# Kernel optimization log

Hardware: AMD Instinct MI355X
Metric: run time of the kernel (lower is better)

The kernel has to match this reference:

```python
import jax, jax.numpy as jnp
import numpy as np

N = 2048   # number of proposals
D = 128    # appearance feature dim
DK = 64    # key/query dim
DG = 64    # geometric embedding dim
SD = 8     # single relation output dim = appear_dim / N_r = 128/16


def setup_inputs() -> dict:
    key = jax.random.key(0)
    ks = jax.random.split(key, 10)
    s = jnp.float32(0.05)
    return {
        "appearance_feature": jax.random.normal(ks[0], (N, D), jnp.float32),
        "geometric_feature": jax.random.uniform(ks[1], (N, N, DG), jnp.float32),
        "Wv": jax.random.normal(ks[2], (D, SD), jnp.float32) * s,
        "bv": jnp.zeros((SD,), jnp.float32),
        "Wk": jax.random.normal(ks[3], (D, DK), jnp.float32) * s,
        "bk": jnp.zeros((DK,), jnp.float32),
        "Wq": jax.random.normal(ks[4], (D, DK), jnp.float32) * s,
        "bq": jnp.zeros((DK,), jnp.float32),
        "Wg": jax.random.normal(ks[5], (DG, 1), jnp.float32) * s,
        "bg": jnp.zeros((1,), jnp.float32),
    }


def reference(appearance_feature, geometric_feature, Wv, bv, Wk, bk, Wq, bq, Wg, bg):
    n = geometric_feature.shape[0]
    # value projection: [N, SD]
    appear = appearance_feature @ Wv + bv
    # key/query projections: [N, DK]
    k = appearance_feature @ Wk + bk
    q = appearance_feature @ Wq + bq
    # appearance attention logits: [N, N]
    w_A = (k @ q.T) * (1.0 / jnp.sqrt(jnp.float32(DK)))
    # geometric gate: relu(W_G(geom)) -> [N, N]
    w_G = jax.nn.relu(
        (geometric_feature.reshape(-1, DG) @ Wg + bg).reshape(n, n)
    )
    # gated exp, normalized over axis 0 (as in the source: torch.sum(w_nominator, 0))
    w_nom = w_G * jnp.exp(w_A)
    w = w_nom / jnp.sum(w_nom, axis=0, keepdims=True)
    # weighted sum of values: [N, SD]
    return w @ appear
```

## Files before the change

kernel.cpp:

```cpp
#include <hip/hip_runtime.h>

#define N 2048
#define D 128
#define DK 64
#define DG 64
#define SD 8
#define TI 32
#define TJ 64

typedef float f4v __attribute__((ext_vector_type(4)));

__global__ __launch_bounds__(128) void proj_kernel(
    const float* __restrict__ A,
    const float* __restrict__ Wv, const float* __restrict__ bv,
    const float* __restrict__ Wk, const float* __restrict__ bk,
    const float* __restrict__ Wq, const float* __restrict__ bq,
    float* __restrict__ kout, float* __restrict__ qout, float* __restrict__ vout)
{
    __shared__ float arow[D];
    const int i = blockIdx.x;
    const int t = threadIdx.x;
    arow[t] = A[(size_t)i * D + t];
    __syncthreads();
    for (int e = t; e < 2 * DK + SD; e += 128) {
        const float* W; const float* b; int od; int col;
        if (e < DK)            { W = Wk; b = bk; od = DK; col = e; }
        else if (e < 2 * DK)   { W = Wq; b = bq; od = DK; col = e - DK; }
        else                   { W = Wv; b = bv; od = SD; col = e - 2 * DK; }
        float acc = 0.f;
        #pragma unroll 8
        for (int c = 0; c < D; ++c) acc += arow[c] * W[c * od + col];
        acc += b[col];
        if (e < DK)          kout[(size_t)i * DK + col] = acc;
        else if (e < 2 * DK) qout[(size_t)i * DK + col] = acc;
        else                 vout[(size_t)i * SD + col] = acc;
    }
}

__global__ __launch_bounds__(256) void expa_kernel(
    const float* __restrict__ kin, const float* __restrict__ qin,
    float* __restrict__ expA)
{
    const int tid = threadIdx.x;
    const int j0 = blockIdx.x * 256;
    const int i0 = blockIdx.y * 16;

    const f4v* qrow = (const f4v*)(qin + (size_t)(j0 + tid) * DK);
    f4v qv[16];
    #pragma unroll
    for (int m = 0; m < 16; ++m) qv[m] = qrow[m];

    const f4v* krow = (const f4v*)(kin + (size_t)i0 * DK);
    #pragma unroll
    for (int r = 0; r < 16; ++r) {
        float p = 0.f;
        #pragma unroll
        for (int m = 0; m < 16; ++m) {
            const f4v kf = krow[r * 16 + m];
            p += kf.x * qv[m].x + kf.y * qv[m].y + kf.z * qv[m].z + kf.w * qv[m].w;
        }
        expA[(size_t)(i0 + r) * N + j0 + tid] = expf(p * 0.125f);
    }
}

__global__ __launch_bounds__(256) void gate_kernel(
    const float* __restrict__ geom,
    const float* __restrict__ Wg, const float* __restrict__ bg,
    float* __restrict__ wbuf,
    float* __restrict__ colpartial)
{
    const int tid = threadIdx.x;
    const int j0 = blockIdx.x * TJ;
    const int i0 = blockIdx.y * TI;
    const int jl = tid >> 2;
    const int c0 = tid & 3;
    const int j  = j0 + jl;
    const float bgv = bg[0];

    f4v wgq[4];
    #pragma unroll
    for (int m = 0; m < 4; ++m) wgq[m] = ((const f4v*)Wg)[c0 + 4 * m];

    float colacc = 0.f;

    #pragma unroll 4
    for (int ii = 0; ii < TI; ++ii) {
        const float* rp = geom + ((size_t)(i0 + ii) * N + j) * DG + c0 * 4;
        const f4v g0 = __builtin_nontemporal_load((const f4v*)(rp));
        const f4v g1 = __builtin_nontemporal_load((const f4v*)(rp + 16));
        const f4v g2 = __builtin_nontemporal_load((const f4v*)(rp + 32));
        const f4v g3 = __builtin_nontemporal_load((const f4v*)(rp + 48));
        float s = g0.x * wgq[0].x + g0.y * wgq[0].y + g0.z * wgq[0].z + g0.w * wgq[0].w
                + g1.x * wgq[1].x + g1.y * wgq[1].y + g1.z * wgq[1].z + g1.w * wgq[1].w
                + g2.x * wgq[2].x + g2.y * wgq[2].y + g2.z * wgq[2].z + g2.w * wgq[2].w
                + g3.x * wgq[3].x + g3.y * wgq[3].y + g3.z * wgq[3].z + g3.w * wgq[3].w;
        s += __shfl_xor(s, 1);
        s += __shfl_xor(s, 2);
        s = fmaxf(s + bgv, 0.f);
        float* wp = wbuf + (size_t)(i0 + ii) * N + j;
        const float val = s * (*wp);
        colacc += val;
        if (c0 == 0) *wp = val;
    }
    if (c0 == 0) colpartial[(size_t)blockIdx.y * N + j] = colacc;
}

__global__ __launch_bounds__(256) void colsum_kernel(
    const float* __restrict__ colpartial, float* __restrict__ colrcp)
{
    const int j = blockIdx.x * 256 + threadIdx.x;
    float acc = 0.f;
    #pragma unroll 8
    for (int r = 0; r < N / TI; ++r) acc += colpartial[(size_t)r * N + j];
    colrcp[j] = 1.0f / acc;
}

__global__ __launch_bounds__(256) void out_kernel(
    const float* __restrict__ w_nom, const float* __restrict__ colrcp,
    const float* __restrict__ appear, float* __restrict__ out)
{
    const int i = blockIdx.x;
    const int t = threadIdx.x;
    float acc[SD];
    #pragma unroll
    for (int s = 0; s < SD; ++s) acc[s] = 0.f;

    #pragma unroll
    for (int jj = 0; jj < N / (256 * 4); ++jj) {
        const int j4 = jj * 256 + t;
        const f4v wn = ((const f4v*)(w_nom + (size_t)i * N))[j4];
        const f4v rc = ((const f4v*)colrcp)[j4];
        const float w0 = wn.x * rc.x, w1 = wn.y * rc.y, w2 = wn.z * rc.z, w3 = wn.w * rc.w;
        const int j = j4 * 4;
        const f4v* a0 = (const f4v*)(appear + (size_t)j * SD);
        f4v r0 = a0[0], r1 = a0[1];
        f4v r2 = a0[2], r3 = a0[3];
        f4v r4 = a0[4], r5 = a0[5];
        f4v r6 = a0[6], r7 = a0[7];
        acc[0] += w0 * r0.x + w1 * r2.x + w2 * r4.x + w3 * r6.x;
        acc[1] += w0 * r0.y + w1 * r2.y + w2 * r4.y + w3 * r6.y;
        acc[2] += w0 * r0.z + w1 * r2.z + w2 * r4.z + w3 * r6.z;
        acc[3] += w0 * r0.w + w1 * r2.w + w2 * r4.w + w3 * r6.w;
        acc[4] += w0 * r1.x + w1 * r3.x + w2 * r5.x + w3 * r7.x;
        acc[5] += w0 * r1.y + w1 * r3.y + w2 * r5.y + w3 * r7.y;
        acc[6] += w0 * r1.z + w1 * r3.z + w2 * r5.z + w3 * r7.z;
        acc[7] += w0 * r1.w + w1 * r3.w + w2 * r5.w + w3 * r7.w;
    }
    #pragma unroll
    for (int s = 0; s < SD; ++s) {
        #pragma unroll
        for (int off = 32; off >= 1; off >>= 1)
            acc[s] += __shfl_down(acc[s], off);
    }
    __shared__ float red[4][SD];
    const int wave = t >> 6;
    const int lane = t & 63;
    if (lane == 0) {
        #pragma unroll
        for (int s = 0; s < SD; ++s) red[wave][s] = acc[s];
    }
    __syncthreads();
    if (t < SD) out[(size_t)i * SD + t] = red[0][t] + red[1][t] + red[2][t] + red[3][t];
}

extern "C" void kernel_launch(void* const* d_in, const int* in_sizes, int n_in,
                              void* d_out, int out_size, void* d_ws, size_t ws_size,
                              hipStream_t stream) {
    const float* A    = (const float*)d_in[0];
    const float* geom = (const float*)d_in[1];
    const float* Wv   = (const float*)d_in[2];
    const float* bv   = (const float*)d_in[3];
    const float* Wk   = (const float*)d_in[4];
    const float* bk   = (const float*)d_in[5];
    const float* Wq   = (const float*)d_in[6];
    const float* bq   = (const float*)d_in[7];
    const float* Wg   = (const float*)d_in[8];
    const float* bg   = (const float*)d_in[9];
    float* out = (float*)d_out;

    float* ws = (float*)d_ws;
    float* kbuf       = ws;
    float* qbuf       = kbuf + (size_t)N * DK;
    float* appear     = qbuf + (size_t)N * DK;
    float* wbuf       = appear + (size_t)N * SD;
    float* colpartial = wbuf + (size_t)N * N;
    float* colrcp     = colpartial + (size_t)(N / TI) * N;

    proj_kernel<<<N, 128, 0, stream>>>(A, Wv, bv, Wk, bk, Wq, bq, kbuf, qbuf, appear);
    expa_kernel<<<dim3(N / 256, N / 16), 256, 0, stream>>>(kbuf, qbuf, wbuf);
    gate_kernel<<<dim3(N / TJ, N / TI), 256, 0, stream>>>(geom, Wg, bg, wbuf, colpartial);
    colsum_kernel<<<N / 256, 256, 0, stream>>>(colpartial, colrcp);
    out_kernel<<<N, 256, 0, stream>>>(wbuf, colrcp, appear, out);
}
```

Before: 298.4 us.

## Restructure gate kernel to per-row contiguous geometry reads with separate column-sum pass

The gate kernel now gives one block a full row i and has each wave stream 64 contiguous geometry vectors (16 f4v loads per lane, fully coalesced), reducing across 16 lanes with shuffles. Results are staged in shared memory so the write-back to the weight row is coalesced. The column partial sums that used to be fused into the gate kernel move into a new colpart kernel that rereads the 16 MB weight matrix, followed by a 16-way reduction kernel. This trades an extra pass over wbuf and one more launch for cleaner streaming of the 1 GB geometry tensor.

```diff
diff --git a/kernel.cpp b/kernel.cpp
--- a/kernel.cpp
+++ b/kernel.cpp
@@ -5,8 +5,7 @@
 #define DK 64
 #define DG 64
 #define SD 8
-#define TI 32
-#define TJ 64
+#define WJ 256
 
 typedef float f4v __attribute__((ext_vector_type(4)));
 
@@ -66,52 +65,65 @@
 __global__ __launch_bounds__(256) void gate_kernel(
     const float* __restrict__ geom,
     const float* __restrict__ Wg, const float* __restrict__ bg,
-    float* __restrict__ wbuf,
-    float* __restrict__ colpartial)
-{
-    const int tid = threadIdx.x;
-    const int j0 = blockIdx.x * TJ;
-    const int i0 = blockIdx.y * TI;
-    const int jl = tid >> 2;
-    const int c0 = tid & 3;
-    const int j  = j0 + jl;
+    float* __restrict__ wbuf)
+{
+    __shared__ float gs[4][64];
+    const int tid  = threadIdx.x;
+    const int i    = blockIdx.x;
+    const int wv   = tid >> 6;
+    const int lane = tid & 63;
+    const int grp  = lane >> 4;
+    const int sub  = lane & 15;
+
+    const f4v wg4  = ((const f4v*)Wg)[sub];
     const float bgv = bg[0];
 
-    f4v wgq[4];
-    #pragma unroll
-    for (int m = 0; m < 4; ++m) wgq[m] = ((const f4v*)Wg)[c0 + 4 * m];
-
-    float colacc = 0.f;
-
-    #pragma unroll 4
-    for (int ii = 0; ii < TI; ++ii) {
-        const float* rp = geom + ((size_t)(i0 + ii) * N + j) * DG + c0 * 4;
-        const f4v g0 = __builtin_nontemporal_load((const f4v*)(rp));
-        const f4v g1 = __builtin_nontemporal_load((const f4v*)(rp + 16));
-        const f4v g2 = __builtin_nontemporal_load((const f4v*)(rp + 32));
-        const f4v g3 = __builtin_nontemporal_load((const f4v*)(rp + 48));
-        float s = g0.x * wgq[0].x + g0.y * wgq[0].y + g0.z * wgq[0].z + g0.w * wgq[0].w
-                + g1.x * wgq[1].x + g1.y * wgq[1].y + g1.z * wgq[1].z + g1.w * wgq[1].w
-                + g2.x * wgq[2].x + g2.y * wgq[2].y + g2.z * wgq[2].z + g2.w * wgq[2].w
-                + g3.x * wgq[3].x + g3.y * wgq[3].y + g3.z * wgq[3].z + g3.w * wgq[3].w;
-        s += __shfl_xor(s, 1);
-        s += __shfl_xor(s, 2);
-        s = fmaxf(s + bgv, 0.f);
-        float* wp = wbuf + (size_t)(i0 + ii) * N + j;
-        const float val = s * (*wp);
-        colacc += val;
-        if (c0 == 0) *wp = val;
-    }
-    if (c0 == 0) colpartial[(size_t)blockIdx.y * N + j] = colacc;
-}
-
-__global__ __launch_bounds__(256) void colsum_kernel(
-    const float* __restrict__ colpartial, float* __restrict__ colrcp)
+    const float* rowbase = geom + (size_t)i * N * DG;
+    float* wrow = wbuf + (size_t)i * N;
+
+    for (int t = 0; t < N / WJ; ++t) {
+        const int jbase = t * WJ + wv * 64;
+        const f4v* src = (const f4v*)(rowbase + (size_t)jbase * DG);
+        f4v gbb[16];
+        #pragma unroll
+        for (int q = 0; q < 16; ++q)
+            gbb[q] = __builtin_nontemporal_load(src + q * 64 + lane);
+        const float ew = wrow[jbase + lane];
+        #pragma unroll
+        for (int q = 0; q < 16; ++q) {
+            float s = gbb[q].x * wg4.x + gbb[q].y * wg4.y
+                    + gbb[q].z * wg4.z + gbb[q].w * wg4.w;
+            s += __shfl_xor(s, 1);
+            s += __shfl_xor(s, 2);
+            s += __shfl_xor(s, 4);
+            s += __shfl_xor(s, 8);
+            s = fmaxf(s + bgv, 0.f);
+            const float e = __shfl(ew, q * 4 + grp);
+            const float val = s * e;
+            if (sub == 0) gs[wv][q * 4 + grp] = val;
+        }
+        wrow[jbase + lane] = gs[wv][lane];
+    }
+}
+
+__global__ __launch_bounds__(256) void colpart_kernel(
+    const float* __restrict__ wbuf, float* __restrict__ colpart)
+{
+    const int j  = blockIdx.x * 256 + threadIdx.x;
+    const int r0 = blockIdx.y * (N / 16);
+    float acc = 0.f;
+    #pragma unroll 8
+    for (int r = 0; r < N / 16; ++r) acc += wbuf[(size_t)(r0 + r) * N + j];
+    colpart[(size_t)blockIdx.y * N + j] = acc;
+}
+
+__global__ __launch_bounds__(256) void colrcp_kernel(
+    const float* __restrict__ colpart, float* __restrict__ colrcp)
 {
     const int j = blockIdx.x * 256 + threadIdx.x;
     float acc = 0.f;
-    #pragma unroll 8
-    for (int r = 0; r < N / TI; ++r) acc += colpartial[(size_t)r * N + j];
+    #pragma unroll
+    for (int r = 0; r < 16; ++r) acc += colpart[(size_t)r * N + j];
     colrcp[j] = 1.0f / acc;
 }
 
@@ -179,16 +191,17 @@
     float* out = (float*)d_out;
 
     float* ws = (float*)d_ws;
-    float* kbuf       = ws;
-    float* qbuf       = kbuf + (size_t)N * DK;
-    float* appear     = qbuf + (size_t)N * DK;
-    float* wbuf       = appear + (size_t)N * SD;
-    float* colpartial = wbuf + (size_t)N * N;
-    float* colrcp     = colpartial + (size_t)(N / TI) * N;
+    float* kbuf    = ws;
+    float* qbuf    = kbuf + (size_t)N * DK;
+    float* appear  = qbuf + (size_t)N * DK;
+    float* wbuf    = appear + (size_t)N * SD;
+    float* colpart = wbuf + (size_t)N * N;
+    float* colrcp  = colpart + (size_t)16 * N;
 
     proj_kernel<<<N, 128, 0, stream>>>(A, Wv, bv, Wk, bk, Wq, bq, kbuf, qbuf, appear);
     expa_kernel<<<dim3(N / 256, N / 16), 256, 0, stream>>>(kbuf, qbuf, wbuf);
-    gate_kernel<<<dim3(N / TJ, N / TI), 256, 0, stream>>>(geom, Wg, bg, wbuf, colpartial);
-    colsum_kernel<<<N / 256, 256, 0, stream>>>(colpartial, colrcp);
+    gate_kernel<<<N, 256, 0, stream>>>(geom, Wg, bg, wbuf);
+    colpart_kernel<<<dim3(N / 256, 16), 256, 0, stream>>>(wbuf, colpart);
+    colrcp_kernel<<<N / 256, 256, 0, stream>>>(colpart, colrcp);
     out_kernel<<<N, 256, 0, stream>>>(wbuf, colrcp, appear, out);
 }
```

New measurement: 273.2 us. -8.4%, faster.
